# Kernel optimization log

Measured on AMD Instinct MI355X. Metric: run time of the kernel, lower is better.

Reference implementation:

```python
import jax, jax.numpy as jnp
import numpy as np

B, N = 256, 4096
IMG_W, IMG_H = 640.0, 480.0


def setup_inputs() -> dict:
    key = jax.random.key(0)
    k0, k1, k2, k3 = jax.random.split(key, 4)
    kpts0 = jax.random.uniform(k0, (B, N, 2), dtype=jnp.float32) * jnp.array([IMG_W, IMG_H], jnp.float32)
    kpts1 = jax.random.uniform(k1, (B, N, 2), dtype=jnp.float32) * jnp.array([IMG_W, IMG_H], jnp.float32)
    conf = jax.random.uniform(k2, (B, N, 1), dtype=jnp.float32)
    t_scale = jax.random.uniform(k3, (B, 2), dtype=jnp.float32) + 0.5
    Kmat = jnp.array([[500.0, 0.0, 320.0], [0.0, 500.0, 240.0], [0.0, 0.0, 1.0]], jnp.float32)
    K = jnp.tile(Kmat[None, None], (B, 2, 1, 1))
    gt_pose_0to1 = jnp.tile(jnp.eye(4, dtype=jnp.float32)[None], (B, 1, 1))
    return {"kpts0": kpts0, "kpts1": kpts1, "conf": conf, "t_scale": t_scale, "K": K, "gt_pose_0to1": gt_pose_0to1}


def _normalize(kpts, Kmat):
    # pixel -> normalized camera coords, homogeneous. kpts:[B,N,2], Kmat:[B,3,3] -> [B,N,3]
    Kinv = jnp.linalg.inv(Kmat)
    h = jnp.concatenate([kpts, jnp.ones_like(kpts[..., :1])], axis=-1)
    return jnp.einsum('bij,bnj->bni', Kinv, h)


def _se3_weighted_8pt(kpts0, kpts1, K0, K1, w, t_scale):
    b_, n_ = kpts0.shape[0], kpts0.shape[1]
    x0 = _normalize(kpts0, K0)  # [B,N,3]
    x1 = _normalize(kpts1, K1)  # [B,N,3]
    # epipolar constraint x1^T E x0 = 0 -> row kron(x1, x0): [B,N,9]
    X = (x1[..., :, None] * x0[..., None, :]).reshape(b_, n_, 9)
    # confidence-weighted normal equations, 9x9 per batch
    M = jnp.einsum('bn,bni,bnj->bij', w, X, X)
    _, V = jnp.linalg.eigh(M)
    E = V[..., 0].reshape(b_, 3, 3)  # eigvec of smallest eigenvalue
    # project to essential manifold + decompose
    U, S, Vt = jnp.linalg.svd(E)
    W = jnp.array([[0.0, -1.0, 0.0], [1.0, 0.0, 0.0], [0.0, 0.0, 1.0]], E.dtype)
    R1 = U @ W @ Vt
    R2 = U @ W.T @ Vt
    R1 = R1 * jnp.sign(jnp.linalg.det(R1))[:, None, None]
    R2 = R2 * jnp.sign(jnp.linalg.det(R2))[:, None, None]
    t = U[..., 2]  # [B,3]
    Rc = jnp.stack([R1, R1, R2, R2], axis=1)   # [B,4,3,3]
    tc = jnp.stack([t, -t, t, -t], axis=1)     # [B,4,3]
    # cheirality: solve d0 * (R x0) - d1 * x1 = -t in least squares (2x2 closed form)
    a = jnp.einsum('bcij,bnj->bcni', Rc, x0)   # [B,4,N,3]
    bvec = x1[:, None]                          # [B,1,N,3]
    tt = tc[:, :, None, :]                      # [B,4,1,3]
    aa = jnp.sum(a * a, -1)
    bb = jnp.sum(bvec * bvec, -1)
    ab = jnp.sum(a * bvec, -1)
    at = jnp.sum(a * tt, -1)
    bt = jnp.sum(bvec * tt, -1)
    det = aa * bb - ab * ab + 1e-9
    d0 = (-at * bb + ab * bt) / det
    d1 = (aa * bt - ab * at) / det
    pos = ((d0 > 0) & (d1 > 0)).astype(w.dtype)
    score = jnp.sum(w[:, None] * pos, -1)       # [B,4]
    best = jnp.argmax(jax.lax.stop_gradient(score), axis=-1)
    oh = jax.nn.one_hot(best, 4, dtype=kpts0.dtype)
    R = jnp.einsum('bc,bcij->bij', oh, Rc)
    t_best = jnp.einsum('bc,bci->bi', oh, tc)
    t_sc = t_best * t_scale[:, None]            # scale unit translation
    top = jnp.concatenate([R, t_sc[..., None]], axis=-1)  # [B,3,4]
    bot = jnp.broadcast_to(jnp.array([0.0, 0.0, 0.0, 1.0], R.dtype), (b_, 1, 4))
    return jnp.concatenate([top, bot], axis=1)  # [B,4,4]


def _se3_inverse(T):
    R = T[:, :3, :3]
    t = T[:, :3, 3:]
    Rt = jnp.swapaxes(R, -1, -2)
    tin = -(Rt @ t)
    top = jnp.concatenate([Rt, tin], axis=-1)
    bot = jnp.broadcast_to(jnp.array([0.0, 0.0, 0.0, 1.0], T.dtype), (T.shape[0], 1, 4))
    return jnp.concatenate([top, bot], axis=1)


def reference(kpts0, kpts1, conf, t_scale, K, gt_pose_0to1):
    w = conf[..., 0]
    T01 = _se3_weighted_8pt(kpts0, kpts1, K[:, 0], K[:, 1], w, t_scale[:, 0])
    T10 = _se3_inverse(T01)
    return jnp.stack([T01, T10], axis=1)  # [B,2,4,4]
```

## Files before the change

### kernel.cpp

```cpp
#include <hip/hip_runtime.h>
#include <math.h>

#define NBATCH 256
#define NPTS   4096
#define NT     512
#define PPT    (NPTS / NT)
#define NWAVE  (NT / 64)

#define IDX(r,c)   ((r)*((r)+1)/2+(c))
#define UPIDX(r,c) ((r)*9 - ((r)*((r)-1))/2 + ((c)-(r)))

__device__ __forceinline__ void inv3x3f(const float* __restrict__ Km, float* Ki) {
  double a = Km[0], bb = Km[1], c = Km[2];
  double d = Km[3], e  = Km[4], f = Km[5];
  double g = Km[6], h  = Km[7], i = Km[8];
  double C00 =  e*i - f*h;
  double C01 = -(d*i - f*g);
  double C02 =  d*h - e*g;
  double det = a*C00 + bb*C01 + c*C02;
  double rd = 1.0/det;
  Ki[0] = (float)(C00*rd); Ki[1] = (float)(-(bb*i - c*h)*rd); Ki[2] = (float)( (bb*f - c*e)*rd);
  Ki[3] = (float)(C01*rd); Ki[4] = (float)( (a*i  - c*g)*rd); Ki[5] = (float)(-(a*f  - c*d)*rd);
  Ki[6] = (float)(C02*rd); Ki[7] = (float)(-(a*h - bb*g)*rd); Ki[8] = (float)( (a*e  - bb*d)*rd);
}

__global__ __launch_bounds__(NT, 1)
void pose_fused(const float* __restrict__ kpts0,
                const float* __restrict__ kpts1,
                const float* __restrict__ conf,
                const float* __restrict__ t_scale,
                const float* __restrict__ Kmat,
                float* __restrict__ out)
{
  const int b    = blockIdx.x;
  const int tid  = threadIdx.x;
  const int lane = tid & 63;
  const int wv   = tid >> 6;

  __shared__ float  red[NWAVE][45];
  __shared__ double sMd[45];
  __shared__ float  sR[21];
  __shared__ float  sscore[NWAVE][4];

  float Ki0[9], Ki1[9];
  inv3x3f(Kmat + (size_t)b*18,     Ki0);
  inv3x3f(Kmat + (size_t)b*18 + 9, Ki1);

  const float2* k0p = (const float2*)kpts0 + (size_t)b*NPTS;
  const float2* k1p = (const float2*)kpts1 + (size_t)b*NPTS;
  const float*  cp  = conf + (size_t)b*NPTS;

  float acc[45];
#pragma unroll
  for (int j=0;j<45;j++) acc[j] = 0.f;

#pragma unroll
  for (int p=0;p<PPT;p++) {
    const int i = tid + p*NT;
    const float2 q0 = k0p[i];
    const float2 q1 = k1p[i];
    const float  w  = cp[i];
    float x0[3], x1[3];
    x0[0] = fmaf(Ki0[0],q0.x, fmaf(Ki0[1],q0.y, Ki0[2]));
    x0[1] = fmaf(Ki0[3],q0.x, fmaf(Ki0[4],q0.y, Ki0[5]));
    x0[2] = fmaf(Ki0[6],q0.x, fmaf(Ki0[7],q0.y, Ki0[8]));
    x1[0] = fmaf(Ki1[0],q1.x, fmaf(Ki1[1],q1.y, Ki1[2]));
    x1[1] = fmaf(Ki1[3],q1.x, fmaf(Ki1[4],q1.y, Ki1[5]));
    x1[2] = fmaf(Ki1[6],q1.x, fmaf(Ki1[7],q1.y, Ki1[8]));
    float X[9], wX[9];
#pragma unroll
    for (int ii=0; ii<3; ii++)
#pragma unroll
      for (int jj=0; jj<3; jj++)
        X[ii*3+jj] = x1[ii]*x0[jj];
#pragma unroll
    for (int j=0;j<9;j++) wX[j] = w*X[j];
    int k = 0;
#pragma unroll
    for (int r=0;r<9;r++)
#pragma unroll
      for (int c=r;c<9;c++) { acc[k] = fmaf(wX[r], X[c], acc[k]); k++; }
  }

#pragma unroll
  for (int j=0;j<45;j++) {
    float v = acc[j];
#pragma unroll
    for (int off=32; off>0; off>>=1) v += __shfl_xor(v, off, 64);
    acc[j] = v;
  }
  if (lane == 0) {
#pragma unroll
    for (int j=0;j<45;j++) red[wv][j] = acc[j];
  }
  __syncthreads();
  if (tid < 45) {
    double s = 0.0;
#pragma unroll
    for (int wq=0; wq<NWAVE; wq++) s += (double)red[wq][tid];
    sMd[tid] = s;
  }
  __syncthreads();

  if (tid == 0) {
    double L[45];
#pragma unroll
    for (int r=0;r<9;r++)
#pragma unroll
      for (int c=0;c<=r;c++)
        L[IDX(r,c)] = sMd[UPIDX(c,r)];

    double dinv[9];
#pragma unroll
    for (int k=0;k<9;k++) {
      double s = L[IDX(k,k)];
#pragma unroll
      for (int j=0;j<k;j++) s -= L[IDX(k,j)]*L[IDX(k,j)];
      double l = sqrt(fmax(s, 1e-30));
      L[IDX(k,k)] = l;
      dinv[k] = 1.0/l;
#pragma unroll
      for (int i2=k+1;i2<9;i2++) {
        double s2 = L[IDX(i2,k)];
#pragma unroll
        for (int j=0;j<k;j++) s2 -= L[IDX(i2,j)]*L[IDX(k,j)];
        L[IDX(i2,k)] = s2*dinv[k];
      }
    }

#pragma unroll
    for (int j=0;j<9;j++) {
#pragma unroll
      for (int i2=j+1;i2<9;i2++) {
        double s = L[IDX(i2,j)]*dinv[j];
#pragma unroll
        for (int k=j+1;k<i2;k++) s += L[IDX(i2,k)]*L[IDX(k,j)];
        L[IDX(i2,j)] = -s*dinv[i2];
      }
    }
#pragma unroll
    for (int j=0;j<9;j++) L[IDX(j,j)] = dinv[j];

#pragma unroll
    for (int i2=0;i2<9;i2++) {
      double tmp[9];
#pragma unroll
      for (int j=0;j<=i2;j++) {
        double s = 0.0;
#pragma unroll
        for (int k=i2;k<9;k++) s += L[IDX(k,i2)]*L[IDX(k,j)];
        tmp[j] = s;
      }
#pragma unroll
      for (int j=0;j<=i2;j++) L[IDX(i2,j)] = tmp[j];
    }

    double v[9];
#pragma unroll
    for (int j=0;j<9;j++) v[j] = 0.125;
    v[4] = 1.0;
    for (int it=0; it<20; it++) {
      double y[9];
#pragma unroll
      for (int i2=0;i2<9;i2++) {
        double s = 0.0;
#pragma unroll
        for (int j=0;j<9;j++) {
          const int rr = (i2>j)?i2:j, cc = (i2>j)?j:i2;
          s = fma(L[IDX(rr,cc)], v[j], s);
        }
        y[i2] = s;
      }
#pragma unroll
      for (int j=0;j<9;j++) v[j] = y[j];
    }
    {
      double nn = 0.0;
#pragma unroll
      for (int j=0;j<9;j++) nn += v[j]*v[j];
      double rn = 1.0/sqrt(nn);
#pragma unroll
      for (int j=0;j<9;j++) v[j] *= rn;
    }

    double E0[3][3];
#pragma unroll
    for (int ii=0;ii<3;ii++)
#pragma unroll
      for (int jj=0;jj<3;jj++) E0[ii][jj] = v[ii*3+jj];
    double G[3][3];
#pragma unroll
    for (int a2=0;a2<3;a2++)
#pragma unroll
      for (int b2=0;b2<3;b2++)
        G[a2][b2] = E0[0][a2]*E0[0][b2] + E0[1][a2]*E0[1][b2] + E0[2][a2]*E0[2][b2];
    double Vv[3][3] = {{1,0,0},{0,1,0},{0,0,1}};
#define JROT(P,Q,RR) do { \
      double apq = G[P][Q]; \
      if (fabs(apq) > 1e-300) { \
        double app = G[P][P], aqq = G[Q][Q]; \
        double tau = (aqq - app) / (2.0*apq); \
        double tt = ((tau >= 0.0) ? 1.0 : -1.0) / (fabs(tau) + sqrt(1.0 + tau*tau)); \
        double cc_ = 1.0/sqrt(1.0 + tt*tt); \
        double ss_ = tt*cc_; \
        G[P][P] = app - tt*apq; \
        G[Q][Q] = aqq + tt*apq; \
        G[P][Q] = 0.0; G[Q][P] = 0.0; \
        double grp = G[RR][P], grq = G[RR][Q]; \
        G[RR][P] = cc_*grp - ss_*grq; G[P][RR] = G[RR][P]; \
        G[RR][Q] = ss_*grp + cc_*grq; G[Q][RR] = G[RR][Q]; \
        double v0p = Vv[0][P], v0q = Vv[0][Q]; \
        Vv[0][P] = cc_*v0p - ss_*v0q; Vv[0][Q] = ss_*v0p + cc_*v0q; \
        double v1p = Vv[1][P], v1q = Vv[1][Q]; \
        Vv[1][P] = cc_*v1p - ss_*v1q; Vv[1][Q] = ss_*v1p + cc_*v1q; \
        double v2p = Vv[2][P], v2q = Vv[2][Q]; \
        Vv[2][P] = cc_*v2p - ss_*v2q; Vv[2][Q] = ss_*v2p + cc_*v2q; \
      } } while(0)
    for (int sw=0; sw<6; sw++) { JROT(0,1,2); JROT(0,2,1); JROT(1,2,0); }
#undef JROT
    double lam[3] = {G[0][0], G[1][1], G[2][2]};
#define CSWAP(A_,B_) if (lam[A_] < lam[B_]) { \
      double tl = lam[A_]; lam[A_] = lam[B_]; lam[B_] = tl; \
      double t0_ = Vv[0][A_]; Vv[0][A_] = Vv[0][B_]; Vv[0][B_] = t0_; \
      double t1_ = Vv[1][A_]; Vv[1][A_] = Vv[1][B_]; Vv[1][B_] = t1_; \
      double t2_ = Vv[2][A_]; Vv[2][A_] = Vv[2][B_]; Vv[2][B_] = t2_; }
    CSWAP(0,1); CSWAP(0,2); CSWAP(1,2);
#undef CSWAP
    double u1[3], u2[3], u3[3];
#pragma unroll
    for (int i3=0;i3<3;i3++)
      u1[i3] = E0[i3][0]*Vv[0][0] + E0[i3][1]*Vv[1][0] + E0[i3][2]*Vv[2][0];
    double n1 = 1.0/sqrt(fmax(u1[0]*u1[0]+u1[1]*u1[1]+u1[2]*u1[2], 1e-300));
#pragma unroll
    for (int i3=0;i3<3;i3++) u1[i3] *= n1;
#pragma unroll
    for (int i3=0;i3<3;i3++)
      u2[i3] = E0[i3][0]*Vv[0][1] + E0[i3][1]*Vv[1][1] + E0[i3][2]*Vv[2][1];
    double d12 = u1[0]*u2[0]+u1[1]*u2[1]+u1[2]*u2[2];
#pragma unroll
    for (int i3=0;i3<3;i3++) u2[i3] -= d12*u1[i3];
    double n2 = 1.0/sqrt(fmax(u2[0]*u2[0]+u2[1]*u2[1]+u2[2]*u2[2], 1e-300));
#pragma unroll
    for (int i3=0;i3<3;i3++) u2[i3] *= n2;
    u3[0] = u1[1]*u2[2] - u1[2]*u2[1];
    u3[1] = u1[2]*u2[0] - u1[0]*u2[2];
    u3[2] = u1[0]*u2[1] - u1[1]*u2[0];
    double R1a[9], R2a[9];
#pragma unroll
    for (int i3=0;i3<3;i3++)
#pragma unroll
      for (int j3=0;j3<3;j3++) {
        double m  = u3[i3]*Vv[j3][2];
        double pA = u2[i3]*Vv[j3][0] - u1[i3]*Vv[j3][1];
        R1a[i3*3+j3] = pA + m;
        R2a[i3*3+j3] = m - pA;
      }
    double det1 = R1a[0]*(R1a[4]*R1a[8]-R1a[5]*R1a[7])
                - R1a[1]*(R1a[3]*R1a[8]-R1a[5]*R1a[6])
                + R1a[2]*(R1a[3]*R1a[7]-R1a[4]*R1a[6]);
    double det2 = R2a[0]*(R2a[4]*R2a[8]-R2a[5]*R2a[7])
                - R2a[1]*(R2a[3]*R2a[8]-R2a[5]*R2a[6])
                + R2a[2]*(R2a[3]*R2a[7]-R2a[4]*R2a[6]);
    double sg1 = (det1 < 0.0) ? -1.0 : 1.0;
    double sg2 = (det2 < 0.0) ? -1.0 : 1.0;
#pragma unroll
    for (int j3=0;j3<9;j3++) { sR[j3] = (float)(sg1*R1a[j3]); sR[9+j3] = (float)(sg2*R2a[j3]); }
    sR[18] = (float)u3[0]; sR[19] = (float)u3[1]; sR[20] = (float)u3[2];
  }
  __syncthreads();

  float r1[9], r2[9], tv[3];
#pragma unroll
  for (int j=0;j<9;j++) { r1[j] = sR[j]; r2[j] = sR[9+j]; }
  tv[0] = sR[18]; tv[1] = sR[19]; tv[2] = sR[20];

  float sc[4] = {0.f, 0.f, 0.f, 0.f};
#pragma unroll
  for (int p=0;p<PPT;p++) {
    const int i = tid + p*NT;
    const float2 q0 = k0p[i];
    const float2 q1 = k1p[i];
    const float  w  = cp[i];
    float x0[3], x1[3];
    x0[0] = fmaf(Ki0[0],q0.x, fmaf(Ki0[1],q0.y, Ki0[2]));
    x0[1] = fmaf(Ki0[3],q0.x, fmaf(Ki0[4],q0.y, Ki0[5]));
    x0[2] = fmaf(Ki0[6],q0.x, fmaf(Ki0[7],q0.y, Ki0[8]));
    x1[0] = fmaf(Ki1[0],q1.x, fmaf(Ki1[1],q1.y, Ki1[2]));
    x1[1] = fmaf(Ki1[3],q1.x, fmaf(Ki1[4],q1.y, Ki1[5]));
    x1[2] = fmaf(Ki1[6],q1.x, fmaf(Ki1[7],q1.y, Ki1[8]));
    const float bb2 = x1[0]*x1[0]+x1[1]*x1[1]+x1[2]*x1[2];
    const float bt  = x1[0]*tv[0]+x1[1]*tv[1]+x1[2]*tv[2];
    {
      float a0 = r1[0]*x0[0]+r1[1]*x0[1]+r1[2]*x0[2];
      float a1 = r1[3]*x0[0]+r1[4]*x0[1]+r1[5]*x0[2];
      float a2 = r1[6]*x0[0]+r1[7]*x0[1]+r1[8]*x0[2];
      float aa = a0*a0+a1*a1+a2*a2;
      float ab = a0*x1[0]+a1*x1[1]+a2*x1[2];
      float at = a0*tv[0]+a1*tv[1]+a2*tv[2];
      float n0v = ab*bt - at*bb2;
      float n1v = aa*bt - ab*at;
      if (n0v > 0.f && n1v > 0.f) sc[0] += w;
      if (n0v < 0.f && n1v < 0.f) sc[1] += w;
    }
    {
      float a0 = r2[0]*x0[0]+r2[1]*x0[1]+r2[2]*x0[2];
      float a1 = r2[3]*x0[0]+r2[4]*x0[1]+r2[5]*x0[2];
      float a2 = r2[6]*x0[0]+r2[7]*x0[1]+r2[8]*x0[2];
      float aa = a0*a0+a1*a1+a2*a2;
      float ab = a0*x1[0]+a1*x1[1]+a2*x1[2];
      float at = a0*tv[0]+a1*tv[1]+a2*tv[2];
      float n0v = ab*bt - at*bb2;
      float n1v = aa*bt - ab*at;
      if (n0v > 0.f && n1v > 0.f) sc[2] += w;
      if (n0v < 0.f && n1v < 0.f) sc[3] += w;
    }
  }
#pragma unroll
  for (int c=0;c<4;c++) {
    float vv = sc[c];
#pragma unroll
    for (int off=32; off>0; off>>=1) vv += __shfl_xor(vv, off, 64);
    sc[c] = vv;
  }
  if (lane == 0) {
#pragma unroll
    for (int c=0;c<4;c++) sscore[wv][c] = sc[c];
  }
  __syncthreads();

  if (tid == 0) {
    float st[4];
#pragma unroll
    for (int c=0;c<4;c++) {
      float s = 0.f;
#pragma unroll
      for (int wq=0; wq<NWAVE; wq++) s += sscore[wq][c];
      st[c] = s;
    }
    int bestc = 0; float bs = st[0];
    if (st[1] > bs) { bs = st[1]; bestc = 1; }
    if (st[2] > bs) { bs = st[2]; bestc = 2; }
    if (st[3] > bs) { bs = st[3]; bestc = 3; }
    float Rb[9];
#pragma unroll
    for (int j=0;j<9;j++) Rb[j] = (bestc < 2) ? r1[j] : r2[j];
    const float sg = (bestc & 1) ? -1.f : 1.f;
    const float ts = t_scale[(size_t)b*2];
    const float t0 = sg*tv[0]*ts, t1 = sg*tv[1]*ts, t2 = sg*tv[2]*ts;
    float* o = out + (size_t)b*32;
    o[0]=Rb[0]; o[1]=Rb[1]; o[2] =Rb[2]; o[3] =t0;
    o[4]=Rb[3]; o[5]=Rb[4]; o[6] =Rb[5]; o[7] =t1;
    o[8]=Rb[6]; o[9]=Rb[7]; o[10]=Rb[8]; o[11]=t2;
    o[12]=0.f; o[13]=0.f; o[14]=0.f; o[15]=1.f;
    const float ti0 = -(Rb[0]*t0 + Rb[3]*t1 + Rb[6]*t2);
    const float ti1 = -(Rb[1]*t0 + Rb[4]*t1 + Rb[7]*t2);
    const float ti2 = -(Rb[2]*t0 + Rb[5]*t1 + Rb[8]*t2);
    o[16]=Rb[0]; o[17]=Rb[3]; o[18]=Rb[6]; o[19]=ti0;
    o[20]=Rb[1]; o[21]=Rb[4]; o[22]=Rb[7]; o[23]=ti1;
    o[24]=Rb[2]; o[25]=Rb[5]; o[26]=Rb[8]; o[27]=ti2;
    o[28]=0.f; o[29]=0.f; o[30]=0.f; o[31]=1.f;
  }
}

extern "C" void kernel_launch(void* const* d_in, const int* in_sizes, int n_in,
                              void* d_out, int out_size, void* d_ws, size_t ws_size,
                              hipStream_t stream) {
  (void)in_sizes; (void)n_in; (void)out_size; (void)d_ws; (void)ws_size;
  const float* kpts0  = (const float*)d_in[0];
  const float* kpts1  = (const float*)d_in[1];
  const float* conf   = (const float*)d_in[2];
  const float* tscale = (const float*)d_in[3];
  const float* K      = (const float*)d_in[4];
  float* outp = (float*)d_out;
  pose_fused<<<dim3(NBATCH), dim3(NT), 0, stream>>>(kpts0, kpts1, conf, tscale, K, outp);
}
```

Baseline: 98.23 us.

## Vectorize point loads and keep normalized points in registers for cheirality pass

Each thread now loads two points per iteration with float4 keypoint and float2 confidence loads instead of float2/float scalar loads. The normalized coordinates and weights are kept in per-thread register arrays, so the second cheirality pass no longer re-reads global memory or recomputes the normalization. In exchange, register pressure rises by about 56 floats per thread alongside the 45 accumulators, which could reduce occupancy or cause spills. The point-to-thread mapping also changes, which alters the order of the float summation.

```diff
diff --git a/kernel.cpp b/kernel.cpp
--- a/kernel.cpp
+++ b/kernel.cpp
@@ -46,40 +46,51 @@
   inv3x3f(Kmat + (size_t)b*18,     Ki0);
   inv3x3f(Kmat + (size_t)b*18 + 9, Ki1);
 
-  const float2* k0p = (const float2*)kpts0 + (size_t)b*NPTS;
-  const float2* k1p = (const float2*)kpts1 + (size_t)b*NPTS;
-  const float*  cp  = conf + (size_t)b*NPTS;
-
+  const float4* k0p4 = (const float4*)(kpts0 + (size_t)b*NPTS*2);
+  const float4* k1p4 = (const float4*)(kpts1 + (size_t)b*NPTS*2);
+  const float2* cp2  = (const float2*)(conf  + (size_t)b*NPTS);
+
+  float px0[PPT][3], px1[PPT][3], pw[PPT];
   float acc[45];
 #pragma unroll
   for (int j=0;j<45;j++) acc[j] = 0.f;
 
 #pragma unroll
-  for (int p=0;p<PPT;p++) {
-    const int i = tid + p*NT;
-    const float2 q0 = k0p[i];
-    const float2 q1 = k1p[i];
-    const float  w  = cp[i];
-    float x0[3], x1[3];
-    x0[0] = fmaf(Ki0[0],q0.x, fmaf(Ki0[1],q0.y, Ki0[2]));
-    x0[1] = fmaf(Ki0[3],q0.x, fmaf(Ki0[4],q0.y, Ki0[5]));
-    x0[2] = fmaf(Ki0[6],q0.x, fmaf(Ki0[7],q0.y, Ki0[8]));
-    x1[0] = fmaf(Ki1[0],q1.x, fmaf(Ki1[1],q1.y, Ki1[2]));
-    x1[1] = fmaf(Ki1[3],q1.x, fmaf(Ki1[4],q1.y, Ki1[5]));
-    x1[2] = fmaf(Ki1[6],q1.x, fmaf(Ki1[7],q1.y, Ki1[8]));
-    float X[9], wX[9];
-#pragma unroll
-    for (int ii=0; ii<3; ii++)
-#pragma unroll
-      for (int jj=0; jj<3; jj++)
-        X[ii*3+jj] = x1[ii]*x0[jj];
-#pragma unroll
-    for (int j=0;j<9;j++) wX[j] = w*X[j];
-    int k = 0;
-#pragma unroll
-    for (int r=0;r<9;r++)
-#pragma unroll
-      for (int c=r;c<9;c++) { acc[k] = fmaf(wX[r], X[c], acc[k]); k++; }
+  for (int p=0;p<PPT/2;p++) {
+    const int idx = tid + p*NT;
+    const float4 q0 = k0p4[idx];
+    const float4 q1 = k1p4[idx];
+    const float2 w2 = cp2[idx];
+#pragma unroll
+    for (int h=0; h<2; h++) {
+      const int pt = 2*p + h;
+      const float u0 = h ? q0.z : q0.x, v0 = h ? q0.w : q0.y;
+      const float u1 = h ? q1.z : q1.x, v1 = h ? q1.w : q1.y;
+      const float w  = h ? w2.y : w2.x;
+      float x0[3], x1[3];
+      x0[0] = fmaf(Ki0[0],u0, fmaf(Ki0[1],v0, Ki0[2]));
+      x0[1] = fmaf(Ki0[3],u0, fmaf(Ki0[4],v0, Ki0[5]));
+      x0[2] = fmaf(Ki0[6],u0, fmaf(Ki0[7],v0, Ki0[8]));
+      x1[0] = fmaf(Ki1[0],u1, fmaf(Ki1[1],v1, Ki1[2]));
+      x1[1] = fmaf(Ki1[3],u1, fmaf(Ki1[4],v1, Ki1[5]));
+      x1[2] = fmaf(Ki1[6],u1, fmaf(Ki1[7],v1, Ki1[8]));
+#pragma unroll
+      for (int j=0;j<3;j++) { px0[pt][j] = x0[j]; px1[pt][j] = x1[j]; }
+      pw[pt] = w;
+      float X[9], wX[9];
+#pragma unroll
+      for (int ii=0; ii<3; ii++)
+#pragma unroll
+        for (int jj=0; jj<3; jj++)
+          X[ii*3+jj] = x1[ii]*x0[jj];
+#pragma unroll
+      for (int j=0;j<9;j++) wX[j] = w*X[j];
+      int k = 0;
+#pragma unroll
+      for (int r=0;r<9;r++)
+#pragma unroll
+        for (int c=r;c<9;c++) { acc[k] = fmaf(wX[r], X[c], acc[k]); k++; }
+    }
   }
 
 #pragma unroll
@@ -277,38 +288,30 @@
   float sc[4] = {0.f, 0.f, 0.f, 0.f};
 #pragma unroll
   for (int p=0;p<PPT;p++) {
-    const int i = tid + p*NT;
-    const float2 q0 = k0p[i];
-    const float2 q1 = k1p[i];
-    const float  w  = cp[i];
-    float x0[3], x1[3];
-    x0[0] = fmaf(Ki0[0],q0.x, fmaf(Ki0[1],q0.y, Ki0[2]));
-    x0[1] = fmaf(Ki0[3],q0.x, fmaf(Ki0[4],q0.y, Ki0[5]));
-    x0[2] = fmaf(Ki0[6],q0.x, fmaf(Ki0[7],q0.y, Ki0[8]));
-    x1[0] = fmaf(Ki1[0],q1.x, fmaf(Ki1[1],q1.y, Ki1[2]));
-    x1[1] = fmaf(Ki1[3],q1.x, fmaf(Ki1[4],q1.y, Ki1[5]));
-    x1[2] = fmaf(Ki1[6],q1.x, fmaf(Ki1[7],q1.y, Ki1[8]));
-    const float bb2 = x1[0]*x1[0]+x1[1]*x1[1]+x1[2]*x1[2];
-    const float bt  = x1[0]*tv[0]+x1[1]*tv[1]+x1[2]*tv[2];
+    const float x00 = px0[p][0], x01 = px0[p][1], x02 = px0[p][2];
+    const float x10 = px1[p][0], x11 = px1[p][1], x12 = px1[p][2];
+    const float w   = pw[p];
+    const float bb2 = x10*x10 + x11*x11 + x12*x12;
+    const float bt  = x10*tv[0] + x11*tv[1] + x12*tv[2];
     {
-      float a0 = r1[0]*x0[0]+r1[1]*x0[1]+r1[2]*x0[2];
-      float a1 = r1[3]*x0[0]+r1[4]*x0[1]+r1[5]*x0[2];
-      float a2 = r1[6]*x0[0]+r1[7]*x0[1]+r1[8]*x0[2];
-      float aa = a0*a0+a1*a1+a2*a2;
-      float ab = a0*x1[0]+a1*x1[1]+a2*x1[2];
-      float at = a0*tv[0]+a1*tv[1]+a2*tv[2];
+      float a0 = r1[0]*x00 + r1[1]*x01 + r1[2]*x02;
+      float a1 = r1[3]*x00 + r1[4]*x01 + r1[5]*x02;
+      float a2 = r1[6]*x00 + r1[7]*x01 + r1[8]*x02;
+      float aa = a0*a0 + a1*a1 + a2*a2;
+      float ab = a0*x10 + a1*x11 + a2*x12;
+      float at = a0*tv[0] + a1*tv[1] + a2*tv[2];
       float n0v = ab*bt - at*bb2;
       float n1v = aa*bt - ab*at;
       if (n0v > 0.f && n1v > 0.f) sc[0] += w;
       if (n0v < 0.f && n1v < 0.f) sc[1] += w;
     }
     {
-      float a0 = r2[0]*x0[0]+r2[1]*x0[1]+r2[2]*x0[2];
-      float a1 = r2[3]*x0[0]+r2[4]*x0[1]+r2[5]*x0[2];
-      float a2 = r2[6]*x0[0]+r2[7]*x0[1]+r2[8]*x0[2];
-      float aa = a0*a0+a1*a1+a2*a2;
-      float ab = a0*x1[0]+a1*x1[1]+a2*x1[2];
-      float at = a0*tv[0]+a1*tv[1]+a2*tv[2];
+      float a0 = r2[0]*x00 + r2[1]*x01 + r2[2]*x02;
+      float a1 = r2[3]*x00 + r2[4]*x01 + r2[5]*x02;
+      float a2 = r2[6]*x00 + r2[7]*x01 + r2[8]*x02;
+      float aa = a0*a0 + a1*a1 + a2*a2;
+      float ab = a0*x10 + a1*x11 + a2*x12;
+      float at = a0*tv[0] + a1*tv[1] + a2*tv[2];
       float n0v = ab*bt - at*bb2;
       float n1v = aa*bt - ab*at;
       if (n0v > 0.f && n1v > 0.f) sc[2] += w;
```

Measured after the change: 97.62 us, median of 2. No clear change (-0.6%).
